# Optimization experiments

Measured on AMD Instinct MI355X. Metric: run time of the kernel, lower is better.

## Reference

```python
import jax, jax.numpy as jnp
import numpy as np

N = 50000      # nodes
E = 800000     # edges
D_IN = 128
D_H = 128
D_OUT = 64


def setup_inputs() -> dict:
    key = jax.random.key(0)
    ks = jax.random.split(key, 10)
    x = jax.random.normal(ks[0], (N, D_IN), dtype=jnp.float32)
    edge_index = jax.random.randint(ks[1], (2, E), 0, N, dtype=jnp.int32)
    def glorot(k, fan_in, fan_out):
        s = jnp.sqrt(6.0 / (fan_in + fan_out)).astype(jnp.float32)
        return jax.random.uniform(k, (fan_in, fan_out), jnp.float32, -s, s)
    return {
        "x": x,
        "edge_index": edge_index,
        "W1": glorot(ks[2], D_IN, D_H), "b1": jnp.zeros((D_H,), jnp.float32),
        "W2": glorot(ks[3], D_H, D_H),  "b2": jnp.zeros((D_H,), jnp.float32),
        "W3": glorot(ks[4], D_H, D_H),  "b3": jnp.zeros((D_H,), jnp.float32),
        "Wfc": glorot(ks[5], D_H, D_OUT), "bfc": jnp.zeros((D_OUT,), jnp.float32),
    }


def gcn_conv(x, W, b, src, dst, n):
    h = x @ W                                   # [N, d_out]
    loop = jnp.arange(n, dtype=src.dtype)
    src_f = jnp.concatenate([src, loop])        # [E+N]
    dst_f = jnp.concatenate([dst, loop])
    deg = jax.ops.segment_sum(jnp.ones_like(dst_f, dtype=h.dtype), dst_f, num_segments=n)
    dinv = jnp.where(deg > 0, jax.lax.rsqrt(deg), 0.0)
    norm = dinv[src_f] * dinv[dst_f]            # [E+N]
    msgs = h[src_f] * norm[:, None]             # gather + scale
    out = jax.ops.segment_sum(msgs, dst_f, num_segments=n)  # scatter-add
    return out + b


def reference(x, edge_index, W1, b1, W2, b2, W3, b3, Wfc, bfc):
    src, dst = edge_index[0], edge_index[1]
    n = x.shape[0]
    h = x
    for W, b in ((W1, b1), (W2, b2), (W3, b3)):
        h = jax.nn.relu(gcn_conv(h, W, b, src, dst, n))
    # dropout is identity in eval mode
    return h @ Wfc + bfc
```

## Files before the change

### kernel.cpp

```cpp
#include <hip/hip_runtime.h>

#define NN 50000
#define EE 800000
#define DD 128
#define DOUTC 64
#define CAP 64
#define BUCKET_BLKS 3125

typedef unsigned int uint;
typedef unsigned short ushort;
typedef __attribute__((ext_vector_type(8))) short bf16x8;
typedef __attribute__((ext_vector_type(4))) float f32x4;

__device__ __forceinline__ float bf2f(uint b) { return __uint_as_float(b << 16); }
__device__ __forceinline__ ushort f2bf(float f) {
    uint u = __float_as_uint(f);
    u += 0x7fffu + ((u >> 16) & 1u);
    return (ushort)(u >> 16);
}

struct PreArgs {
    const float *w1, *w2, *w3, *wfc;
    ushort *wt1, *wt2, *wt3, *wtfc;
    int* cnt;
};

__global__ __launch_bounds__(256) void k_pre(PreArgs a) {
    int b = blockIdx.x, t = threadIdx.x;
    if (b < 196) {
        int i = b * 256 + t;
        if (i < NN) a.cnt[i] = 0;
    } else if (b < 388) {
        int b2 = b - 196;
        const float* w = (b2 < 64) ? a.w1 : (b2 < 128) ? a.w2 : a.w3;
        ushort* wt = (b2 < 64) ? a.wt1 : (b2 < 128) ? a.wt2 : a.wt3;
        int idx = (b2 & 63) * 256 + t;
        int k = idx >> 7, n = idx & 127;
        wt[n * DD + k] = f2bf(w[idx]);
    } else {
        int idx = (b - 388) * 256 + t;
        int k = idx >> 6, n = idx & 63;
        a.wtfc[n * DD + k] = f2bf(a.wfc[idx]);
    }
}


__global__ __launch_bounds__(256) void k_front(
    const int* __restrict__ src, const int* __restrict__ dst,
    int* __restrict__ cnt, ushort* __restrict__ colb,
    const float* __restrict__ X, const ushort* __restrict__ WT1,
    ushort* __restrict__ T) {
    int b = blockIdx.x;
    if (b < BUCKET_BLKS) {
        int e = b * 256 + threadIdx.x;
        int d = dst[e];
        int s = src[e];
        int p = atomicAdd(&cnt[d], 1);
        if (p < CAP) colb[((size_t)d << 6) + p] = (ushort)s;
        return;
    }
    const int mb = b - BUCKET_BLKS;
    const int wave = threadIdx.x >> 6;
    const int lane = threadIdx.x & 63;
    const int m0w = mb * 64 + wave * 16;
    if (m0w >= NN) return;
    const int m = m0w + (lane & 15);
    const int quad = lane >> 4;
    f32x4 acc[8];
#pragma unroll
    for (int nt = 0; nt < 8; ++nt) acc[nt] = (f32x4){0.f, 0.f, 0.f, 0.f};
    const float* Hrow = X + (size_t)m * DD;
#pragma unroll
    for (int kk = 0; kk < 4; ++kk) {
        float4 a0 = *(const float4*)(Hrow + kk * 32 + quad * 8);
        float4 a1 = *(const float4*)(Hrow + kk * 32 + quad * 8 + 4);
        bf16x8 bfr;
        bfr[0] = (short)f2bf(a0.x); bfr[1] = (short)f2bf(a0.y);
        bfr[2] = (short)f2bf(a0.z); bfr[3] = (short)f2bf(a0.w);
        bfr[4] = (short)f2bf(a1.x); bfr[5] = (short)f2bf(a1.y);
        bfr[6] = (short)f2bf(a1.z); bfr[7] = (short)f2bf(a1.w);
#pragma unroll
        for (int nt = 0; nt < 8; ++nt) {
            bf16x8 afr = *(const bf16x8*)(WT1 + (size_t)(nt * 16 + (lane & 15)) * DD +
                                          kk * 32 + quad * 8);
            acc[nt] = __builtin_amdgcn_mfma_f32_16x16x32_bf16(afr, bfr, acc[nt], 0, 0, 0);
        }
    }
#pragma unroll
    for (int nt = 0; nt < 8; ++nt) {
        int n = nt * 16 + quad * 4;
        uint2 o;
        o.x = (uint)f2bf(acc[nt][0]) | ((uint)f2bf(acc[nt][1]) << 16);
        o.y = (uint)f2bf(acc[nt][2]) | ((uint)f2bf(acc[nt][3]) << 16);
        *(uint2*)(T + (size_t)m * DD + n) = o;
    }
}

__global__ __launch_bounds__(256) void k_mm(
    const ushort* __restrict__ H, const ushort* __restrict__ WT,
    ushort* __restrict__ T) {
    const int wave = threadIdx.x >> 6;
    const int lane = threadIdx.x & 63;
    const int m0w = blockIdx.x * 64 + wave * 16;
    if (m0w >= NN) return;
    const int m = m0w + (lane & 15);
    const int quad = lane >> 4;
    f32x4 acc[8];
#pragma unroll
    for (int nt = 0; nt < 8; ++nt) acc[nt] = (f32x4){0.f, 0.f, 0.f, 0.f};
    const ushort* Hrow = H + (size_t)m * DD;
#pragma unroll
    for (int kk = 0; kk < 4; ++kk) {
        bf16x8 bfr = *(const bf16x8*)(Hrow + kk * 32 + quad * 8);
#pragma unroll
        for (int nt = 0; nt < 8; ++nt) {
            bf16x8 afr = *(const bf16x8*)(WT + (size_t)(nt * 16 + (lane & 15)) * DD +
                                          kk * 32 + quad * 8);
            acc[nt] = __builtin_amdgcn_mfma_f32_16x16x32_bf16(afr, bfr, acc[nt], 0, 0, 0);
        }
    }
#pragma unroll
    for (int nt = 0; nt < 8; ++nt) {
        int n = nt * 16 + quad * 4;
        uint2 o;
        o.x = (uint)f2bf(acc[nt][0]) | ((uint)f2bf(acc[nt][1]) << 16);
        o.y = (uint)f2bf(acc[nt][2]) | ((uint)f2bf(acc[nt][3]) << 16);
        *(uint2*)(T + (size_t)m * DD + n) = o;
    }
}

__global__ __launch_bounds__(256) void k_agg(
    const ushort* __restrict__ T, const int* __restrict__ cnt,
    const ushort* __restrict__ colb, const float* __restrict__ bias,
    ushort* __restrict__ A) {
    int node = blockIdx.x * 4 + (threadIdx.x >> 6);
    if (node >= NN) return;
    int lane = threadIdx.x & 63;
    const uint* Tv = (const uint*)T;
    size_t base = (size_t)node * 64;
    int c = cnt[node];
    float di = rsqrtf((float)(c + 1));
    uint w0 = Tv[base + lane];
    float ax = di * bf2f(w0 & 0xffffu), ay = di * bf2f(w0 >> 16);
    int end = c < CAP ? c : CAP;
    const ushort* bl = colb + ((size_t)node << 6);
    int e = 0;
    for (; e + 3 < end; e += 4) {
        int s0 = bl[e], s1 = bl[e + 1], s2 = bl[e + 2], s3 = bl[e + 3];
        float d0 = rsqrtf((float)(cnt[s0] + 1));
        float d1 = rsqrtf((float)(cnt[s1] + 1));
        float d2 = rsqrtf((float)(cnt[s2] + 1));
        float d3 = rsqrtf((float)(cnt[s3] + 1));
        uint v0 = Tv[(size_t)s0 * 64 + lane];
        uint v1 = Tv[(size_t)s1 * 64 + lane];
        uint v2 = Tv[(size_t)s2 * 64 + lane];
        uint v3 = Tv[(size_t)s3 * 64 + lane];
        ax = fmaf(d0, bf2f(v0 & 0xffffu), ax);
        ay = fmaf(d0, bf2f(v0 >> 16), ay);
        ax = fmaf(d1, bf2f(v1 & 0xffffu), ax);
        ay = fmaf(d1, bf2f(v1 >> 16), ay);
        ax = fmaf(d2, bf2f(v2 & 0xffffu), ax);
        ay = fmaf(d2, bf2f(v2 >> 16), ay);
        ax = fmaf(d3, bf2f(v3 & 0xffffu), ax);
        ay = fmaf(d3, bf2f(v3 >> 16), ay);
    }
    for (; e < end; ++e) {
        int s = bl[e];
        float dj = rsqrtf((float)(cnt[s] + 1));
        uint v = Tv[(size_t)s * 64 + lane];
        ax = fmaf(dj, bf2f(v & 0xffffu), ax);
        ay = fmaf(dj, bf2f(v >> 16), ay);
    }
    float2 bv = ((const float2*)bias)[lane];
    float o0 = fmaxf(fmaf(ax, di, bv.x), 0.f);
    float o1 = fmaxf(fmaf(ay, di, bv.y), 0.f);
    ((uint*)A)[base + lane] = (uint)f2bf(o0) | ((uint)f2bf(o1) << 16);
}

__global__ __launch_bounds__(256) void k_mm_final(
    const ushort* __restrict__ H, const ushort* __restrict__ WT,
    const float* __restrict__ bb, float* __restrict__ out) {
    const int wave = threadIdx.x >> 6;
    const int lane = threadIdx.x & 63;
    const int m0w = blockIdx.x * 64 + wave * 16;
    if (m0w >= NN) return;
    const int m = m0w + (lane & 15);
    const int quad = lane >> 4;
    f32x4 acc[4];
#pragma unroll
    for (int nt = 0; nt < 4; ++nt) acc[nt] = (f32x4){0.f, 0.f, 0.f, 0.f};
    const ushort* Hrow = H + (size_t)m * DD;
#pragma unroll
    for (int kk = 0; kk < 4; ++kk) {
        bf16x8 bfr = *(const bf16x8*)(Hrow + kk * 32 + quad * 8);
#pragma unroll
        for (int nt = 0; nt < 4; ++nt) {
            bf16x8 afr = *(const bf16x8*)(WT + (size_t)(nt * 16 + (lane & 15)) * DD +
                                          kk * 32 + quad * 8);
            acc[nt] = __builtin_amdgcn_mfma_f32_16x16x32_bf16(afr, bfr, acc[nt], 0, 0, 0);
        }
    }
#pragma unroll
    for (int nt = 0; nt < 4; ++nt) {
        int n = nt * 16 + quad * 4;
        float4 bvals = *(const float4*)(bb + n);
        float4 o = {acc[nt][0] + bvals.x, acc[nt][1] + bvals.y,
                    acc[nt][2] + bvals.z, acc[nt][3] + bvals.w};
        *(float4*)(out + (size_t)m * DOUTC + n) = o;
    }
}

extern "C" void kernel_launch(void* const* d_in, const int* in_sizes, int n_in,
                              void* d_out, int out_size, void* d_ws, size_t ws_size,
                              hipStream_t stream) {
    const float* x   = (const float*)d_in[0];
    const int*   ei  = (const int*)d_in[1];
    const float* W1  = (const float*)d_in[2];
    const float* b1  = (const float*)d_in[3];
    const float* W2  = (const float*)d_in[4];
    const float* b2  = (const float*)d_in[5];
    const float* W3  = (const float*)d_in[6];
    const float* b3  = (const float*)d_in[7];
    const float* Wfc = (const float*)d_in[8];
    const float* bfc = (const float*)d_in[9];

    char* ws = (char*)d_ws;
    size_t off = 0;
    auto take = [&](size_t bytes) {
        void* p = ws + off;
        off = (off + bytes + 255) & ~(size_t)255;
        return p;
    };
    int*    cnt  = (int*)take((size_t)NN * 4);
    ushort* colb = (ushort*)take((size_t)NN * CAP * 2);
    ushort* T    = (ushort*)take((size_t)NN * DD * 2);
    ushort* A    = (ushort*)take((size_t)NN * DD * 2);
    ushort* WT1  = (ushort*)take((size_t)DD * DD * 2);
    ushort* WT2  = (ushort*)take((size_t)DD * DD * 2);
    ushort* WT3  = (ushort*)take((size_t)DD * DD * 2);
    ushort* WTfc = (ushort*)take((size_t)DOUTC * DD * 2);

    const int* src = ei;
    const int* dst = ei + EE;

    PreArgs pa;
    pa.w1 = W1; pa.w2 = W2; pa.w3 = W3; pa.wfc = Wfc;
    pa.wt1 = WT1; pa.wt2 = WT2; pa.wt3 = WT3; pa.wtfc = WTfc;
    pa.cnt = cnt;
    k_pre<<<420, 256, 0, stream>>>(pa);

    const int mm_grid  = (NN + 63) / 64;
    const int agg_grid = (NN + 3) / 4;

    k_front<<<BUCKET_BLKS + mm_grid, 256, 0, stream>>>(src, dst, cnt, colb, x, WT1, T);
    k_agg<<<agg_grid, 256, 0, stream>>>(T, cnt, colb, b1, A);
    k_mm<<<mm_grid, 256, 0, stream>>>(A, WT2, T);
    k_agg<<<agg_grid, 256, 0, stream>>>(T, cnt, colb, b2, A);
    k_mm<<<mm_grid, 256, 0, stream>>>(A, WT3, T);
    k_agg<<<agg_grid, 256, 0, stream>>>(T, cnt, colb, b3, A);
    k_mm_final<<<mm_grid, 256, 0, stream>>>(A, WTfc, bfc, (float*)d_out);
}
```

Measured before the change: 352.2 us.

## Prescale features by source degree in GEMM epilogue, co-locate counts with buckets

Multiplies each GEMM output row by its own rsqrt degree, so the aggregation becomes a plain sum with no per-neighbor count lookups or rsqrt. The count and neighbor list now share one 128-byte row per node, and the gather loop is unrolled by 8 to keep more loads in flight. The bucketing kernel is split off from the first GEMM, which now needs the counts, so the overlap between the two is lost. Zeroing the whole 6.4 MB bucket array costs more than zeroing the old count array, and capacity drops from 64 to 62 neighbors per node.

```diff
diff --git a/kernel.cpp b/kernel.cpp
--- a/kernel.cpp
+++ b/kernel.cpp
@@ -4,8 +4,10 @@
 #define EE 800000
 #define DD 128
 #define DOUTC 64
-#define CAP 64
+#define SLOTS 62
+#define ROWB 128
 #define BUCKET_BLKS 3125
+#define ZERO_BLKS 1563
 
 typedef unsigned int uint;
 typedef unsigned short ushort;
@@ -22,47 +24,45 @@
 struct PreArgs {
     const float *w1, *w2, *w3, *wfc;
     ushort *wt1, *wt2, *wt3, *wtfc;
-    int* cnt;
+    char* colb;
 };
 
 __global__ __launch_bounds__(256) void k_pre(PreArgs a) {
     int b = blockIdx.x, t = threadIdx.x;
-    if (b < 196) {
-        int i = b * 256 + t;
-        if (i < NN) a.cnt[i] = 0;
-    } else if (b < 388) {
-        int b2 = b - 196;
+    if (b < ZERO_BLKS) {
+        size_t i = ((size_t)b * 256 + t) * 16;
+        if (i < (size_t)NN * ROWB) *(uint4*)(a.colb + i) = (uint4){0, 0, 0, 0};
+    } else if (b < ZERO_BLKS + 192) {
+        int b2 = b - ZERO_BLKS;
         const float* w = (b2 < 64) ? a.w1 : (b2 < 128) ? a.w2 : a.w3;
         ushort* wt = (b2 < 64) ? a.wt1 : (b2 < 128) ? a.wt2 : a.wt3;
         int idx = (b2 & 63) * 256 + t;
         int k = idx >> 7, n = idx & 127;
         wt[n * DD + k] = f2bf(w[idx]);
     } else {
-        int idx = (b - 388) * 256 + t;
+        int idx = (b - ZERO_BLKS - 192) * 256 + t;
         int k = idx >> 6, n = idx & 63;
         a.wtfc[n * DD + k] = f2bf(a.wfc[idx]);
     }
 }
 
-
-__global__ __launch_bounds__(256) void k_front(
+__global__ __launch_bounds__(256) void k_bucket(
     const int* __restrict__ src, const int* __restrict__ dst,
-    int* __restrict__ cnt, ushort* __restrict__ colb,
-    const float* __restrict__ X, const ushort* __restrict__ WT1,
-    ushort* __restrict__ T) {
-    int b = blockIdx.x;
-    if (b < BUCKET_BLKS) {
-        int e = b * 256 + threadIdx.x;
-        int d = dst[e];
-        int s = src[e];
-        int p = atomicAdd(&cnt[d], 1);
-        if (p < CAP) colb[((size_t)d << 6) + p] = (ushort)s;
-        return;
-    }
-    const int mb = b - BUCKET_BLKS;
+    char* __restrict__ colb) {
+    int e = blockIdx.x * 256 + threadIdx.x;
+    int d = dst[e];
+    int s = src[e];
+    char* row = colb + ((size_t)d << 7);
+    int p = atomicAdd((int*)row, 1);
+    if (p < SLOTS) *(ushort*)(row + 4 + 2 * p) = (ushort)s;
+}
+
+__global__ __launch_bounds__(256) void k_mm1(
+    const float* __restrict__ X, const ushort* __restrict__ WT,
+    const char* __restrict__ colb, ushort* __restrict__ T) {
     const int wave = threadIdx.x >> 6;
     const int lane = threadIdx.x & 63;
-    const int m0w = mb * 64 + wave * 16;
+    const int m0w = blockIdx.x * 64 + wave * 16;
     if (m0w >= NN) return;
     const int m = m0w + (lane & 15);
     const int quad = lane >> 4;
@@ -81,24 +81,26 @@
         bfr[6] = (short)f2bf(a1.z); bfr[7] = (short)f2bf(a1.w);
 #pragma unroll
         for (int nt = 0; nt < 8; ++nt) {
-            bf16x8 afr = *(const bf16x8*)(WT1 + (size_t)(nt * 16 + (lane & 15)) * DD +
+            bf16x8 afr = *(const bf16x8*)(WT + (size_t)(nt * 16 + (lane & 15)) * DD +
                                           kk * 32 + quad * 8);
             acc[nt] = __builtin_amdgcn_mfma_f32_16x16x32_bf16(afr, bfr, acc[nt], 0, 0, 0);
         }
     }
+    int c = *(const int*)(colb + ((size_t)m << 7));
+    float di = rsqrtf((float)(c + 1));
 #pragma unroll
     for (int nt = 0; nt < 8; ++nt) {
         int n = nt * 16 + quad * 4;
         uint2 o;
-        o.x = (uint)f2bf(acc[nt][0]) | ((uint)f2bf(acc[nt][1]) << 16);
-        o.y = (uint)f2bf(acc[nt][2]) | ((uint)f2bf(acc[nt][3]) << 16);
+        o.x = (uint)f2bf(acc[nt][0] * di) | ((uint)f2bf(acc[nt][1] * di) << 16);
+        o.y = (uint)f2bf(acc[nt][2] * di) | ((uint)f2bf(acc[nt][3] * di) << 16);
         *(uint2*)(T + (size_t)m * DD + n) = o;
     }
 }
 
 __global__ __launch_bounds__(256) void k_mm(
     const ushort* __restrict__ H, const ushort* __restrict__ WT,
-    ushort* __restrict__ T) {
+    const char* __restrict__ colb, ushort* __restrict__ T) {
     const int wave = threadIdx.x >> 6;
     const int lane = threadIdx.x & 63;
     const int m0w = blockIdx.x * 64 + wave * 16;
@@ -119,58 +121,49 @@
             acc[nt] = __builtin_amdgcn_mfma_f32_16x16x32_bf16(afr, bfr, acc[nt], 0, 0, 0);
         }
     }
+    int c = *(const int*)(colb + ((size_t)m << 7));
+    float di = rsqrtf((float)(c + 1));
 #pragma unroll
     for (int nt = 0; nt < 8; ++nt) {
         int n = nt * 16 + quad * 4;
         uint2 o;
-        o.x = (uint)f2bf(acc[nt][0]) | ((uint)f2bf(acc[nt][1]) << 16);
-        o.y = (uint)f2bf(acc[nt][2]) | ((uint)f2bf(acc[nt][3]) << 16);
+        o.x = (uint)f2bf(acc[nt][0] * di) | ((uint)f2bf(acc[nt][1] * di) << 16);
+        o.y = (uint)f2bf(acc[nt][2] * di) | ((uint)f2bf(acc[nt][3] * di) << 16);
         *(uint2*)(T + (size_t)m * DD + n) = o;
     }
 }
 
 __global__ __launch_bounds__(256) void k_agg(
-    const ushort* __restrict__ T, const int* __restrict__ cnt,
-    const ushort* __restrict__ colb, const float* __restrict__ bias,
-    ushort* __restrict__ A) {
+    const ushort* __restrict__ T, const char* __restrict__ colb,
+    const float* __restrict__ bias, ushort* __restrict__ A) {
     int node = blockIdx.x * 4 + (threadIdx.x >> 6);
     if (node >= NN) return;
     int lane = threadIdx.x & 63;
     const uint* Tv = (const uint*)T;
     size_t base = (size_t)node * 64;
-    int c = cnt[node];
+    const char* row = colb + ((size_t)node << 7);
+    int c = *(const int*)row;
+    int end = c < SLOTS ? c : SLOTS;
+    const ushort* bl = (const ushort*)(row + 4);
+    uint w0 = Tv[base + lane];
+    float ax = bf2f(w0 & 0xffffu), ay = bf2f(w0 >> 16);
+    int e = 0;
+    for (; e + 7 < end; e += 8) {
+        uint vv[8];
+#pragma unroll
+        for (int q = 0; q < 8; ++q) vv[q] = Tv[(size_t)bl[e + q] * 64 + lane];
+#pragma unroll
+        for (int q = 0; q < 8; ++q) {
+            ax += bf2f(vv[q] & 0xffffu);
+            ay += bf2f(vv[q] >> 16);
+        }
+    }
+    for (; e < end; ++e) {
+        uint v = Tv[(size_t)bl[e] * 64 + lane];
+        ax += bf2f(v & 0xffffu);
+        ay += bf2f(v >> 16);
+    }
     float di = rsqrtf((float)(c + 1));
-    uint w0 = Tv[base + lane];
-    float ax = di * bf2f(w0 & 0xffffu), ay = di * bf2f(w0 >> 16);
-    int end = c < CAP ? c : CAP;
-    const ushort* bl = colb + ((size_t)node << 6);
-    int e = 0;
-    for (; e + 3 < end; e += 4) {
-        int s0 = bl[e], s1 = bl[e + 1], s2 = bl[e + 2], s3 = bl[e + 3];
-        float d0 = rsqrtf((float)(cnt[s0] + 1));
-        float d1 = rsqrtf((float)(cnt[s1] + 1));
-        float d2 = rsqrtf((float)(cnt[s2] + 1));
-        float d3 = rsqrtf((float)(cnt[s3] + 1));
-        uint v0 = Tv[(size_t)s0 * 64 + lane];
-        uint v1 = Tv[(size_t)s1 * 64 + lane];
-        uint v2 = Tv[(size_t)s2 * 64 + lane];
-        uint v3 = Tv[(size_t)s3 * 64 + lane];
-        ax = fmaf(d0, bf2f(v0 & 0xffffu), ax);
-        ay = fmaf(d0, bf2f(v0 >> 16), ay);
-        ax = fmaf(d1, bf2f(v1 & 0xffffu), ax);
-        ay = fmaf(d1, bf2f(v1 >> 16), ay);
-        ax = fmaf(d2, bf2f(v2 & 0xffffu), ax);
-        ay = fmaf(d2, bf2f(v2 >> 16), ay);
-        ax = fmaf(d3, bf2f(v3 & 0xffffu), ax);
-        ay = fmaf(d3, bf2f(v3 >> 16), ay);
-    }
-    for (; e < end; ++e) {
-        int s = bl[e];
-        float dj = rsqrtf((float)(cnt[s] + 1));
-        uint v = Tv[(size_t)s * 64 + lane];
-        ax = fmaf(dj, bf2f(v & 0xffffu), ax);
-        ay = fmaf(dj, bf2f(v >> 16), ay);
-    }
     float2 bv = ((const float2*)bias)[lane];
     float o0 = fmaxf(fmaf(ax, di, bv.x), 0.f);
     float o1 = fmaxf(fmaf(ay, di, bv.y), 0.f);
@@ -231,8 +224,7 @@
         off = (off + bytes + 255) & ~(size_t)255;
         return p;
     };
-    int*    cnt  = (int*)take((size_t)NN * 4);
-    ushort* colb = (ushort*)take((size_t)NN * CAP * 2);
+    char*   colb = (char*)take((size_t)NN * ROWB);
     ushort* T    = (ushort*)take((size_t)NN * DD * 2);
     ushort* A    = (ushort*)take((size_t)NN * DD * 2);
     ushort* WT1  = (ushort*)take((size_t)DD * DD * 2);
@@ -246,17 +238,18 @@
     PreArgs pa;
     pa.w1 = W1; pa.w2 = W2; pa.w3 = W3; pa.wfc = Wfc;
     pa.wt1 = WT1; pa.wt2 = WT2; pa.wt3 = WT3; pa.wtfc = WTfc;
-    pa.cnt = cnt;
-    k_pre<<<420, 256, 0, stream>>>(pa);
+    pa.colb = colb;
+    k_pre<<<ZERO_BLKS + 192 + 32, 256, 0, stream>>>(pa);
 
     const int mm_grid  = (NN + 63) / 64;
     const int agg_grid = (NN + 3) / 4;
 
-    k_front<<<BUCKET_BLKS + mm_grid, 256, 0, stream>>>(src, dst, cnt, colb, x, WT1, T);
-    k_agg<<<agg_grid, 256, 0, stream>>>(T, cnt, colb, b1, A);
-    k_mm<<<mm_grid, 256, 0, stream>>>(A, WT2, T);
-    k_agg<<<agg_grid, 256, 0, stream>>>(T, cnt, colb, b2, A);
-    k_mm<<<mm_grid, 256, 0, stream>>>(A, WT3, T);
-    k_agg<<<agg_grid, 256, 0, stream>>>(T, cnt, colb, b3, A);
+    k_bucket<<<BUCKET_BLKS, 256, 0, stream>>>(src, dst, colb);
+    k_mm1<<<mm_grid, 256, 0, stream>>>(x, WT1, colb, T);
+    k_agg<<<agg_grid, 256, 0, stream>>>(T, colb, b1, A);
+    k_mm<<<mm_grid, 256, 0, stream>>>(A, WT2, colb, T);
+    k_agg<<<agg_grid, 256, 0, stream>>>(T, colb, b2, A);
+    k_mm<<<mm_grid, 256, 0, stream>>>(A, WT3, colb, T);
+    k_agg<<<agg_grid, 256, 0, stream>>>(T, colb, b3, A);
     k_mm_final<<<mm_grid, 256, 0, stream>>>(A, WTfc, bfc, (float*)d_out);
 }
```

Result: faster. 327.2 us (-7.1%).
